# Optimization experiments

Measured on AMD Instinct MI355X. Metric: run time of the kernel, lower is better.

The kernel has to match this reference:

```python
import jax, jax.numpy as jnp
import numpy as np

N_GAUSS = 3200          # 20*20*8 voxel-center pseudo points
FEAT_DIM = 17
RENDER_H, RENDER_W = 48, 88
GT_H, GT_W = 192, 352
VOXEL_SIZE = 0.8
PC_MIN = np.array([-8.0, -8.0, -3.2], np.float32)
PC_MAX = np.array([8.0, 8.0, 3.2], np.float32)
NUSC_FREQ = np.array([1163161, 2309034, 188743, 2997643, 20317180, 852476, 243808,
                      2457947, 497017, 2731022, 7224789, 214411435, 5565043,
                      63191967, 76098082, 128860031, 141625221, 2307405309], np.float64)


def setup_inputs() -> dict:
    key = jax.random.key(0)
    k1, k2 = jax.random.split(key, 2)
    # pseudo voxel-center grid (get_presudo_xyz): cell centers on a 20x20x8 grid
    gx = (np.arange(20) + 0.5) * VOXEL_SIZE + PC_MIN[0]
    gy = (np.arange(20) + 0.5) * VOXEL_SIZE + PC_MIN[1]
    gz = (np.arange(8) + 0.5) * VOXEL_SIZE + PC_MIN[2]
    X, Y, Z = np.meshgrid(gx, gy, gz, indexing='ij')
    pc_xyz = np.stack([X, Y, Z], -1).reshape(-1, 3).astype(np.float32)
    # distCUDA2 on a regular grid: mean sq dist to 3 NNs == voxel_size^2
    scales = np.full((N_GAUSS, 3), np.log(VOXEL_SIZE), np.float32)  # log(sqrt(v^2))
    rots = np.zeros((N_GAUSS, 4), np.float32); rots[:, 0] = 1.0  # identity quats
    # two cameras looking at the grid (z_cam > 0 for all points)
    vm0 = np.array([[1, 0, 0, 0], [0, -1, 0, 0], [0, 0, -1, 20], [0, 0, 0, 1]], np.float32)
    vm1 = np.array([[0, 1, 0, 0], [0, 0, -1, 0], [-1, 0, 0, 20], [0, 0, 0, 1]], np.float32)
    viewmats = np.stack([vm0, vm1])
    intr = np.array([[100.0, 50.0, RENDER_W / 2.0, RENDER_H / 2.0]] * 2, np.float32)
    cw = (1.0 / np.log(NUSC_FREQ[:17] + 0.001)).astype(np.float32)
    return {
        'voxel_feats': jax.random.normal(k1, (1, N_GAUSS, FEAT_DIM), jnp.float32),
        'opacity': jax.random.uniform(k2, (1, N_GAUSS, 1), jnp.float32),
        'pc_xyz': jnp.asarray(pc_xyz),
        'scales': jnp.asarray(scales),
        'rots': jnp.asarray(rots),
        'viewmats': jnp.asarray(viewmats),
        'intrinsics': jnp.asarray(intr),
        'class_weights': jnp.asarray(cw),
        'gt_sem': jax.random.randint(jax.random.fold_in(key, 1), (2, GT_H, GT_W), 0, 17, jnp.int32),
        'sem_mask': jax.random.randint(jax.random.fold_in(key, 2), (2, GT_H, GT_W), 0, 2, jnp.int32),
    }


def quat_to_rot(q):
    q = q / jnp.linalg.norm(q, axis=-1, keepdims=True)
    w, x, y, z = q[:, 0], q[:, 1], q[:, 2], q[:, 3]
    return jnp.stack([
        jnp.stack([1 - 2 * (y * y + z * z), 2 * (x * y - w * z), 2 * (x * z + w * y)], -1),
        jnp.stack([2 * (x * y + w * z), 1 - 2 * (x * x + z * z), 2 * (y * z - w * x)], -1),
        jnp.stack([2 * (x * z - w * y), 2 * (y * z + w * x), 1 - 2 * (x * x + y * y)], -1),
    ], -2)  # [N,3,3]


def nearest_resize(img, H, W):
    hi, wi = img.shape
    ri = (jnp.arange(H) * hi) // H
    ci = (jnp.arange(W) * wi) // W
    return img[ri][:, ci]


def render_feature_map(feats, opac, xyz, scale, Rq, viewmat, intr):
    fx, fy, cx, cy = intr[0], intr[1], intr[2], intr[3]
    Rw, t = viewmat[:3, :3], viewmat[:3, 3]
    p = xyz @ Rw.T + t                      # [N,3] camera-frame
    z = p[:, 2]
    valid = z > 0.2
    zc = jnp.maximum(z, 0.2)
    u = fx * p[:, 0] / zc + cx
    v = fy * p[:, 1] / zc + cy
    # 3D covariance: Rq diag(s^2) Rq^T, then to camera frame
    cov3d = jnp.einsum('nij,nj,nkj->nik', Rq, scale * scale, Rq)
    cov_c = jnp.einsum('ij,njk,lk->nil', Rw, cov3d, Rw)
    # projection Jacobian (EWA splatting)
    zero = jnp.zeros_like(zc)
    J = jnp.stack([
        jnp.stack([fx / zc, zero, -fx * p[:, 0] / (zc * zc)], -1),
        jnp.stack([zero, fy / zc, -fy * p[:, 1] / (zc * zc)], -1),
    ], -2)                                  # [N,2,3]
    cov2 = jnp.einsum('nij,njk,nlk->nil', J, cov_c, J)
    a = cov2[:, 0, 0] + 0.3
    b = cov2[:, 0, 1]
    c = cov2[:, 1, 1] + 0.3
    det = jnp.maximum(a * c - b * b, 1e-8)
    A, B, C = c / det, -b / det, a / det    # conic
    px = jnp.arange(RENDER_W, dtype=jnp.float32)
    py = jnp.arange(RENDER_H, dtype=jnp.float32)
    dx = px[None, :] - u[:, None]           # [N,W]
    dy = py[None, :] - v[:, None]           # [N,H]
    power = (-0.5 * (A[:, None, None] * dx[:, None, :] ** 2
                     + C[:, None, None] * dy[:, :, None] ** 2)
             - B[:, None, None] * dx[:, None, :] * dy[:, :, None])  # [N,H,W]
    power = jnp.minimum(power, 0.0)
    alpha = jnp.clip(opac[:, None, None] * jnp.exp(power), 0.0, 0.99)
    alpha = alpha * valid[:, None, None].astype(alpha.dtype)
    order = jnp.argsort(z)                  # front-to-back depth sort
    alpha = alpha[order]
    feats_s = feats[order]
    T = jnp.cumprod(1.0 - alpha, axis=0)
    T_excl = jnp.concatenate([jnp.ones_like(T[:1]), T[:-1]], axis=0)
    w = alpha * T_excl                      # composite weights [N,H,W]
    return jnp.einsum('nhw,nc->hwc', w, feats_s)  # [H,W,17]


def masked_weighted_ce(logits, gt, mask, cw):
    logp = jax.nn.log_softmax(logits, -1)
    nll = -jnp.take_along_axis(logp, gt[:, None], axis=1)[:, 0]
    wi = cw[gt] * mask
    return jnp.sum(wi * nll) / jnp.maximum(jnp.sum(wi), 1e-8)


def reference(voxel_feats, opacity, pc_xyz, scales, rots, viewmats, intrinsics,
              class_weights, gt_sem, sem_mask):
    scale = jnp.exp(scales)
    Rq = quat_to_rot(rots)
    B = voxel_feats.shape[0]
    n_cam = viewmats.shape[0]
    loss_batch = 0.0
    for b in range(B):
        feats = voxel_feats[b].reshape(-1, FEAT_DIM)
        opac = opacity[b].reshape(-1)
        loss_cam = 0.0
        for c in range(n_cam):
            img = render_feature_map(feats, opac, pc_xyz, scale, Rq,
                                     viewmats[c], intrinsics[c])
            logits = img.reshape(-1, FEAT_DIM)
            gt = nearest_resize(gt_sem[c], RENDER_H, RENDER_W).reshape(-1)
            m = nearest_resize(sem_mask[c], RENDER_H, RENDER_W).reshape(-1).astype(jnp.float32)
            loss_cam = loss_cam + masked_weighted_ce(logits, gt, m, class_weights)
        loss_batch = loss_batch + loss_cam / n_cam
    return loss_batch / B  # gaussian_sem_weight = 1.0
```

## Files before the change

kernel.cpp:

```cpp
#include <hip/hip_runtime.h>

#define NG 3200
#define NF 17
#define NFP 18
#define RH 48
#define RW 88
#define NPIX (RH*RW)
#define GTH 192
#define GTW 352
#define NCAM 2
#define CHUNK 80
#define NCHUNK 40
#define NPL 9
#define CPW 5
#define NLOSSBLK (NPIX/64*NCAM)

typedef float v2f __attribute__((ext_vector_type(2)));
typedef _Float16 h2 __attribute__((ext_vector_type(2)));

#define Z_OFF    0
#define PU_OFF   (Z_OFF + NCAM*NG)
#define PS_OFF   (PU_OFF + NCAM*NG*6)
#define FS_OFF   (PS_OFF + NCAM*NG*6)
#define PT_OFF   (FS_OFF + NCAM*NG*NFP)
#define ACC_OFF  (PT_OFF + NCAM*NCHUNK*NPL*NPIX)

__global__ __launch_bounds__(256) void k_preproc(
    const float* __restrict__ opac, const float* __restrict__ xyz,
    const float* __restrict__ scales, const float* __restrict__ rots,
    const float* __restrict__ vm, const float* __restrict__ intr,
    float* __restrict__ ws)
{
  int idx = blockIdx.x*blockDim.x + threadIdx.x;
  if (idx < 8) ws[ACC_OFF + idx] = 0.0f;
  if (idx >= NCAM*NG) return;
  int cam = idx / NG, g = idx % NG;

  float qw=rots[g*4+0], qx=rots[g*4+1], qy=rots[g*4+2], qz=rots[g*4+3];
  float qn = rsqrtf(qw*qw+qx*qx+qy*qy+qz*qz);
  qw*=qn; qx*=qn; qy*=qn; qz*=qn;
  float R[3][3];
  R[0][0]=1.f-2.f*(qy*qy+qz*qz); R[0][1]=2.f*(qx*qy-qw*qz); R[0][2]=2.f*(qx*qz+qw*qy);
  R[1][0]=2.f*(qx*qy+qw*qz); R[1][1]=1.f-2.f*(qx*qx+qz*qz); R[1][2]=2.f*(qy*qz-qw*qx);
  R[2][0]=2.f*(qx*qz-qw*qy); R[2][1]=2.f*(qy*qz+qw*qx); R[2][2]=1.f-2.f*(qx*qx+qy*qy);

  float s2[3];
  #pragma unroll
  for (int k=0;k<3;k++){ float s=expf(scales[g*3+k]); s2[k]=s*s; }

  float M[3][3];
  #pragma unroll
  for(int i=0;i<3;i++)
    #pragma unroll
    for(int j=0;j<3;j++)
      M[i][j] = R[i][0]*s2[0]*R[j][0] + R[i][1]*s2[1]*R[j][1] + R[i][2]*s2[2]*R[j][2];

  const float* Vm = vm + cam*16;
  float Rw[3][3], t[3];
  #pragma unroll
  for(int i=0;i<3;i++){
    #pragma unroll
    for(int j=0;j<3;j++) Rw[i][j]=Vm[i*4+j];
    t[i]=Vm[i*4+3];
  }

  float T1[3][3];
  #pragma unroll
  for(int i=0;i<3;i++)
    #pragma unroll
    for(int j=0;j<3;j++)
      T1[i][j] = Rw[i][0]*M[0][j] + Rw[i][1]*M[1][j] + Rw[i][2]*M[2][j];
  float V[3][3];
  #pragma unroll
  for(int i=0;i<3;i++)
    #pragma unroll
    for(int j=0;j<3;j++)
      V[i][j] = T1[i][0]*Rw[j][0] + T1[i][1]*Rw[j][1] + T1[i][2]*Rw[j][2];

  float X=xyz[g*3+0], Y=xyz[g*3+1], Zp=xyz[g*3+2];
  float p0 = Rw[0][0]*X + Rw[0][1]*Y + Rw[0][2]*Zp + t[0];
  float p1 = Rw[1][0]*X + Rw[1][1]*Y + Rw[1][2]*Zp + t[1];
  float p2 = Rw[2][0]*X + Rw[2][1]*Y + Rw[2][2]*Zp + t[2];

  float z  = p2;
  float zc = fmaxf(z, 0.2f);
  float fx=intr[cam*4+0], fy=intr[cam*4+1], cx=intr[cam*4+2], cy=intr[cam*4+3];
  float u = fx*p0/zc + cx;
  float v = fy*p1/zc + cy;

  float j00 = fx/zc, j02 = -fx*p0/(zc*zc);
  float j11 = fy/zc, j12 = -fy*p1/(zc*zc);
  float c00 = j00*j00*V[0][0] + 2.f*j00*j02*V[0][2] + j02*j02*V[2][2];
  float c01 = j00*(V[0][1]*j11 + V[0][2]*j12) + j02*(V[2][1]*j11 + V[2][2]*j12);
  float c11 = j11*j11*V[1][1] + 2.f*j11*j12*V[1][2] + j12*j12*V[2][2];

  float a = c00 + 0.3f, b = c01, c = c11 + 0.3f;
  float det = fmaxf(a*c - b*b, 1e-8f);
  const float L2E = 1.4426950408889634f;
  float A2 = -0.5f*L2E * (c/det);
  float B2 = -L2E * (-b/det);
  float C2 = -0.5f*L2E * (a/det);
  float opv = (z > 0.2f) ? opac[g] : 0.0f;

  ws[Z_OFF + idx] = z;
  float* P = ws + PU_OFF + (size_t)idx*6;
  P[0]=u; P[1]=v; P[2]=A2; P[3]=B2; P[4]=C2; P[5]=opv;
}

__global__ __launch_bounds__(256) void k_sort(
    const float* __restrict__ feats, float* __restrict__ ws)
{
  __shared__ float zsh[NG];
  int cam = blockIdx.y;
  for (int i=threadIdx.x; i<NG; i+=256) zsh[i] = ws[Z_OFF + cam*NG + i];
  __syncthreads();

  int wave = threadIdx.x >> 6, lane = threadIdx.x & 63;
  int g = blockIdx.x*4 + wave;
  float zi = zsh[g];
  int rank = 0;
  #pragma unroll 5
  for (int k=0; k<NG/64; k++){
    int j = k*64 + lane;
    float zj = zsh[j];
    rank += ((zj < zi) || (zj == zi && j < g)) ? 1 : 0;
  }
  #pragma unroll
  for (int off=32; off>0; off>>=1) rank += __shfl_down(rank, off, 64);
  rank = __shfl(rank, 0, 64);

  const float* src = ws + PU_OFF + (size_t)(cam*NG+g)*6;
  if (lane < 6) (ws + PS_OFF + (size_t)(cam*NG+rank)*6)[lane] = src[lane];
  if (lane < NFP) (ws + FS_OFF + (size_t)(cam*NG+rank)*NFP)[lane] =
                     (lane < NF) ? feats[g*NF+lane] : 0.0f;
}

__global__ __launch_bounds__(192) void k_render(float* __restrict__ ws)
{
  __shared__ float sp[CHUNK*6];
  __shared__ v2f   sf2[CHUNK*(NFP/2)];
  int cam = blockIdx.z, chunk = blockIdx.y;
  int g0 = chunk*CHUNK;
  const float* psrc = ws + PS_OFF + (size_t)(cam*NG+g0)*6;
  for (int i=threadIdx.x; i<CHUNK*6; i+=192) sp[i]=psrc[i];
  const float* fsrc = ws + FS_OFF + (size_t)(cam*NG+g0)*NFP;
  float* sff = (float*)sf2;
  for (int i=threadIdx.x; i<CHUNK*NFP; i+=192) sff[i]=fsrc[i];
  __syncthreads();

  int pix = blockIdx.x*192 + threadIdx.x;
  float px = (float)(pix % RW), py = (float)(pix / RW);

  float T = 1.0f;
  v2f F2[9];
  #pragma unroll
  for(int k=0;k<9;k++) F2[k]=(v2f)(0.f);

  #pragma unroll 4
  for (int g=0; g<CHUNK; g++){
    const float* P = sp + g*6;
    float dx = px - P[0], dy = py - P[1];
    float m1 = P[2]*dx;
    float m2 = fmaf(P[3], dy, m1);
    float m3 = dx*m2;
    float power2 = fmaf(P[4]*dy, dy, m3);
    power2 = fminf(power2, 0.f);
    float alpha = fminf(P[5]*exp2f(power2), 0.99f);
    float w = alpha*T;
    T = fmaf(-alpha, T, T);
    v2f w2; w2.x = w; w2.y = w;
    const v2f* f2 = sf2 + g*(NFP/2);
    #pragma unroll
    for(int k=0;k<9;k++) F2[k] += w2*f2[k];
  }

  const float* Ff = (const float*)F2;
  h2* out = (h2*)(ws + PT_OFF) + (size_t)((cam*NCHUNK+chunk)*NPL)*NPIX + pix;
  #pragma unroll
  for(int k=0;k<8;k++){
    h2 v; v.x = (_Float16)Ff[2*k]; v.y = (_Float16)Ff[2*k+1];
    out[k*NPIX] = v;
  }
  { h2 v; v.x = (_Float16)Ff[16]; v.y = (_Float16)T; out[8*NPIX] = v; }
}

__global__ __launch_bounds__(512) void k_loss(
    const int* __restrict__ gt, const int* __restrict__ mask,
    const float* __restrict__ cw, float* __restrict__ ws, float* __restrict__ out)
{
  __shared__ float part[8*64*19];
  int cam = blockIdx.y;
  int wave = threadIdx.x >> 6, lane = threadIdx.x & 63;
  int pix = blockIdx.x*64 + lane;

  float F[NF];
  #pragma unroll
  for(int k=0;k<NF;k++) F[k]=0.f;
  float T = 1.f;
  #pragma unroll
  for (int i=0;i<CPW;i++){
    int c = wave*CPW + i;
    const h2* base = (const h2*)(ws + PT_OFF) + (size_t)((cam*NCHUNK+c)*NPL)*NPIX + pix;
    h2 v[9];
    #pragma unroll
    for(int k=0;k<9;k++) v[k] = base[k*NPIX];
    #pragma unroll
    for(int k=0;k<8;k++){ F[2*k] += T*(float)v[k].x; F[2*k+1] += T*(float)v[k].y; }
    F[16] += T*(float)v[8].x;
    T *= (float)v[8].y;
  }
  float* p = part + (wave*64 + lane)*19;
  #pragma unroll
  for(int k=0;k<NF;k++) p[k]=F[k];
  p[17]=T;
  __syncthreads();

  if (wave == 0){
    float img[NF];
    #pragma unroll
    for(int k=0;k<NF;k++) img[k]=0.f;
    float Trun = 1.f;
    for (int w=0; w<8; w++){
      const float* b = part + (w*64 + lane)*19;
      #pragma unroll
      for(int k=0;k<NF;k++) img[k] += Trun*b[k];
      Trun *= b[17];
    }
    int row = pix / RW, col = pix % RW;
    int gofs = cam*GTH*GTW + (row*4)*GTW + col*4;
    int gi = gt[gofs];
    float mi = (float)mask[gofs];
    float mx = img[0];
    #pragma unroll
    for(int k=1;k<NF;k++) mx = fmaxf(mx, img[k]);
    float s = 0.f;
    #pragma unroll
    for(int k=0;k<NF;k++) s += expf(img[k]-mx);
    float lse = mx + logf(s);
    float nll = lse - img[gi];
    float wi  = cw[gi]*mi;
    float num = wi*nll, den = wi;
    #pragma unroll
    for (int off=32; off>0; off>>=1){
      num += __shfl_down(num, off, 64);
      den += __shfl_down(den, off, 64);
    }
    if (lane == 0){
      atomicAdd(ws + ACC_OFF + cam*2 + 0, num);
      atomicAdd(ws + ACC_OFF + cam*2 + 1, den);
      __threadfence();
      int ticket = (int)atomicAdd(ws + ACC_OFF + 4, 1.0f);
      if (ticket == NLOSSBLK-1){
        float n0 = atomicAdd(ws + ACC_OFF + 0, 0.f);
        float d0 = atomicAdd(ws + ACC_OFF + 1, 0.f);
        float n1 = atomicAdd(ws + ACC_OFF + 2, 0.f);
        float d1 = atomicAdd(ws + ACC_OFF + 3, 0.f);
        float l0 = n0/fmaxf(d0, 1e-8f);
        float l1 = n1/fmaxf(d1, 1e-8f);
        out[0] = 0.5f*(l0 + l1);
      }
    }
  }
}

extern "C" void kernel_launch(void* const* d_in, const int* in_sizes, int n_in,
                              void* d_out, int out_size, void* d_ws, size_t ws_size,
                              hipStream_t stream) {
  const float* vf   = (const float*)d_in[0];
  const float* op   = (const float*)d_in[1];
  const float* xyz  = (const float*)d_in[2];
  const float* sc   = (const float*)d_in[3];
  const float* rt   = (const float*)d_in[4];
  const float* vm   = (const float*)d_in[5];
  const float* intr = (const float*)d_in[6];
  const float* cw   = (const float*)d_in[7];
  const int*   gt   = (const int*)d_in[8];
  const int*   mask = (const int*)d_in[9];
  float* ws  = (float*)d_ws;
  float* out = (float*)d_out;

  k_preproc<<<dim3((NCAM*NG+255)/256), 256, 0, stream>>>(op, xyz, sc, rt, vm, intr, ws);
  k_sort   <<<dim3(NG/4, NCAM), 256, 0, stream>>>(vf, ws);
  k_render <<<dim3(NPIX/192, NCHUNK, NCAM), 192, 0, stream>>>(ws);
  k_loss   <<<dim3(NPIX/64, NCAM), 512, 0, stream>>>(gt, mask, cw, ws, out);
}
```

Baseline: 125.9 us.

## Fuse preprocess into sort, add wave-level gaussian skip, repack partial records

Merges the per-gaussian projection kernel into the depth-sort kernel, which recomputes z in shared memory, so one launch and one workspace round trip go away. The render kernel now uses 40-gaussian chunks (80 chunks), float4 shared loads with padded layouts, and skips a gaussian when every lane in the wave has an exponent below -20. Per-pixel partial results are stored as contiguous 48-byte fp16 records instead of planar planes, and the loss kernel reduces 10 chunks per wave. The skip threshold drops contributions with alpha up to about 1e-6, a slight approximation. The larger chunk count doubles the partial-result traffic.

```diff
diff --git a/kernel.cpp b/kernel.cpp
--- a/kernel.cpp
+++ b/kernel.cpp
@@ -2,117 +2,50 @@
 
 #define NG 3200
 #define NF 17
-#define NFP 18
 #define RH 48
 #define RW 88
 #define NPIX (RH*RW)
 #define GTH 192
 #define GTW 352
 #define NCAM 2
-#define CHUNK 80
-#define NCHUNK 40
-#define NPL 9
-#define CPW 5
+#define CHUNK 40
+#define NCHUNK 80
+#define CPW 10
 #define NLOSSBLK (NPIX/64*NCAM)
-
-typedef float v2f __attribute__((ext_vector_type(2)));
+#define PREC 12
+
+typedef float v4f __attribute__((ext_vector_type(4)));
 typedef _Float16 h2 __attribute__((ext_vector_type(2)));
 
-#define Z_OFF    0
-#define PU_OFF   (Z_OFF + NCAM*NG)
-#define PS_OFF   (PU_OFF + NCAM*NG*6)
-#define FS_OFF   (PS_OFF + NCAM*NG*6)
-#define PT_OFF   (FS_OFF + NCAM*NG*NFP)
-#define ACC_OFF  (PT_OFF + NCAM*NCHUNK*NPL*NPIX)
-
-__global__ __launch_bounds__(256) void k_preproc(
-    const float* __restrict__ opac, const float* __restrict__ xyz,
-    const float* __restrict__ scales, const float* __restrict__ rots,
-    const float* __restrict__ vm, const float* __restrict__ intr,
-    float* __restrict__ ws)
-{
-  int idx = blockIdx.x*blockDim.x + threadIdx.x;
-  if (idx < 8) ws[ACC_OFF + idx] = 0.0f;
-  if (idx >= NCAM*NG) return;
-  int cam = idx / NG, g = idx % NG;
-
-  float qw=rots[g*4+0], qx=rots[g*4+1], qy=rots[g*4+2], qz=rots[g*4+3];
-  float qn = rsqrtf(qw*qw+qx*qx+qy*qy+qz*qz);
-  qw*=qn; qx*=qn; qy*=qn; qz*=qn;
-  float R[3][3];
-  R[0][0]=1.f-2.f*(qy*qy+qz*qz); R[0][1]=2.f*(qx*qy-qw*qz); R[0][2]=2.f*(qx*qz+qw*qy);
-  R[1][0]=2.f*(qx*qy+qw*qz); R[1][1]=1.f-2.f*(qx*qx+qz*qz); R[1][2]=2.f*(qy*qz-qw*qx);
-  R[2][0]=2.f*(qx*qz-qw*qy); R[2][1]=2.f*(qy*qz+qw*qx); R[2][2]=1.f-2.f*(qx*qx+qy*qy);
-
-  float s2[3];
-  #pragma unroll
-  for (int k=0;k<3;k++){ float s=expf(scales[g*3+k]); s2[k]=s*s; }
-
-  float M[3][3];
-  #pragma unroll
-  for(int i=0;i<3;i++)
-    #pragma unroll
-    for(int j=0;j<3;j++)
-      M[i][j] = R[i][0]*s2[0]*R[j][0] + R[i][1]*s2[1]*R[j][1] + R[i][2]*s2[2]*R[j][2];
-
-  const float* Vm = vm + cam*16;
-  float Rw[3][3], t[3];
-  #pragma unroll
-  for(int i=0;i<3;i++){
-    #pragma unroll
-    for(int j=0;j<3;j++) Rw[i][j]=Vm[i*4+j];
-    t[i]=Vm[i*4+3];
-  }
-
-  float T1[3][3];
-  #pragma unroll
-  for(int i=0;i<3;i++)
-    #pragma unroll
-    for(int j=0;j<3;j++)
-      T1[i][j] = Rw[i][0]*M[0][j] + Rw[i][1]*M[1][j] + Rw[i][2]*M[2][j];
-  float V[3][3];
-  #pragma unroll
-  for(int i=0;i<3;i++)
-    #pragma unroll
-    for(int j=0;j<3;j++)
-      V[i][j] = T1[i][0]*Rw[j][0] + T1[i][1]*Rw[j][1] + T1[i][2]*Rw[j][2];
-
-  float X=xyz[g*3+0], Y=xyz[g*3+1], Zp=xyz[g*3+2];
-  float p0 = Rw[0][0]*X + Rw[0][1]*Y + Rw[0][2]*Zp + t[0];
-  float p1 = Rw[1][0]*X + Rw[1][1]*Y + Rw[1][2]*Zp + t[1];
-  float p2 = Rw[2][0]*X + Rw[2][1]*Y + Rw[2][2]*Zp + t[2];
-
-  float z  = p2;
-  float zc = fmaxf(z, 0.2f);
-  float fx=intr[cam*4+0], fy=intr[cam*4+1], cx=intr[cam*4+2], cy=intr[cam*4+3];
-  float u = fx*p0/zc + cx;
-  float v = fy*p1/zc + cy;
-
-  float j00 = fx/zc, j02 = -fx*p0/(zc*zc);
-  float j11 = fy/zc, j12 = -fy*p1/(zc*zc);
-  float c00 = j00*j00*V[0][0] + 2.f*j00*j02*V[0][2] + j02*j02*V[2][2];
-  float c01 = j00*(V[0][1]*j11 + V[0][2]*j12) + j02*(V[2][1]*j11 + V[2][2]*j12);
-  float c11 = j11*j11*V[1][1] + 2.f*j11*j12*V[1][2] + j12*j12*V[2][2];
-
-  float a = c00 + 0.3f, b = c01, c = c11 + 0.3f;
-  float det = fmaxf(a*c - b*b, 1e-8f);
-  const float L2E = 1.4426950408889634f;
-  float A2 = -0.5f*L2E * (c/det);
-  float B2 = -L2E * (-b/det);
-  float C2 = -0.5f*L2E * (a/det);
-  float opv = (z > 0.2f) ? opac[g] : 0.0f;
-
-  ws[Z_OFF + idx] = z;
-  float* P = ws + PU_OFF + (size_t)idx*6;
-  P[0]=u; P[1]=v; P[2]=A2; P[3]=B2; P[4]=C2; P[5]=opv;
-}
-
-__global__ __launch_bounds__(256) void k_sort(
-    const float* __restrict__ feats, float* __restrict__ ws)
+#define PS_OFF   0
+#define FS_OFF   (PS_OFF + NCAM*NG*8)
+#define PT_OFF   (FS_OFF + NCAM*NG*20)
+#define ACC_OFF  (PT_OFF + NCAM*NCHUNK*NPIX*PREC)
+
+__device__ __forceinline__ unsigned pack_h2(float a, float b){
+  h2 r; r.x=(_Float16)a; r.y=(_Float16)b;
+  unsigned u; __builtin_memcpy(&u,&r,4); return u;
+}
+__device__ __forceinline__ void unpack_h2(unsigned u, float& a, float& b){
+  h2 r; __builtin_memcpy(&r,&u,4);
+  a=(float)r.x; b=(float)r.y;
+}
+
+__global__ __launch_bounds__(256) void k_prep_sort(
+    const float* __restrict__ vf, const float* __restrict__ opac,
+    const float* __restrict__ xyz, const float* __restrict__ scales,
+    const float* __restrict__ rots, const float* __restrict__ vm,
+    const float* __restrict__ intr, float* __restrict__ ws)
 {
   __shared__ float zsh[NG];
   int cam = blockIdx.y;
-  for (int i=threadIdx.x; i<NG; i+=256) zsh[i] = ws[Z_OFF + cam*NG + i];
+  const float* Vm = vm + cam*16;
+  {
+    float r20=Vm[8], r21=Vm[9], r22=Vm[10], t2c=Vm[11];
+    for (int i=threadIdx.x; i<NG; i+=256)
+      zsh[i] = fmaf(r20, xyz[i*3], fmaf(r21, xyz[i*3+1], fmaf(r22, xyz[i*3+2], t2c)));
+  }
+  if (blockIdx.x==0 && blockIdx.y==0 && threadIdx.x<8) ws[ACC_OFF+threadIdx.x]=0.f;
   __syncthreads();
 
   int wave = threadIdx.x >> 6, lane = threadIdx.x & 63;
@@ -129,59 +62,123 @@
   for (int off=32; off>0; off>>=1) rank += __shfl_down(rank, off, 64);
   rank = __shfl(rank, 0, 64);
 
-  const float* src = ws + PU_OFF + (size_t)(cam*NG+g)*6;
-  if (lane < 6) (ws + PS_OFF + (size_t)(cam*NG+rank)*6)[lane] = src[lane];
-  if (lane < NFP) (ws + FS_OFF + (size_t)(cam*NG+rank)*NFP)[lane] =
-                     (lane < NF) ? feats[g*NF+lane] : 0.0f;
+  float qw=rots[g*4+0], qx=rots[g*4+1], qy=rots[g*4+2], qz=rots[g*4+3];
+  float qn = rsqrtf(qw*qw+qx*qx+qy*qy+qz*qz);
+  qw*=qn; qx*=qn; qy*=qn; qz*=qn;
+  float R[3][3];
+  R[0][0]=1.f-2.f*(qy*qy+qz*qz); R[0][1]=2.f*(qx*qy-qw*qz); R[0][2]=2.f*(qx*qz+qw*qy);
+  R[1][0]=2.f*(qx*qy+qw*qz); R[1][1]=1.f-2.f*(qx*qx+qz*qz); R[1][2]=2.f*(qy*qz-qw*qx);
+  R[2][0]=2.f*(qx*qz-qw*qy); R[2][1]=2.f*(qy*qz+qw*qx); R[2][2]=1.f-2.f*(qx*qx+qy*qy);
+
+  float s2[3];
+  #pragma unroll
+  for (int k=0;k<3;k++){ float s=expf(scales[g*3+k]); s2[k]=s*s; }
+
+  float M[3][3];
+  #pragma unroll
+  for(int i=0;i<3;i++)
+    #pragma unroll
+    for(int j=0;j<3;j++)
+      M[i][j] = R[i][0]*s2[0]*R[j][0] + R[i][1]*s2[1]*R[j][1] + R[i][2]*s2[2]*R[j][2];
+
+  float Rw[3][3], t[3];
+  #pragma unroll
+  for(int i=0;i<3;i++){
+    #pragma unroll
+    for(int j=0;j<3;j++) Rw[i][j]=Vm[i*4+j];
+    t[i]=Vm[i*4+3];
+  }
+  float T1[3][3];
+  #pragma unroll
+  for(int i=0;i<3;i++)
+    #pragma unroll
+    for(int j=0;j<3;j++)
+      T1[i][j] = Rw[i][0]*M[0][j] + Rw[i][1]*M[1][j] + Rw[i][2]*M[2][j];
+  float V[3][3];
+  #pragma unroll
+  for(int i=0;i<3;i++)
+    #pragma unroll
+    for(int j=0;j<3;j++)
+      V[i][j] = T1[i][0]*Rw[j][0] + T1[i][1]*Rw[j][1] + T1[i][2]*Rw[j][2];
+
+  float X=xyz[g*3+0], Y=xyz[g*3+1], Zp=xyz[g*3+2];
+  float p0 = Rw[0][0]*X + Rw[0][1]*Y + Rw[0][2]*Zp + t[0];
+  float p1 = Rw[1][0]*X + Rw[1][1]*Y + Rw[1][2]*Zp + t[1];
+
+  float z  = zi;
+  float zc = fmaxf(z, 0.2f);
+  float fx=intr[cam*4+0], fy=intr[cam*4+1], cx=intr[cam*4+2], cy=intr[cam*4+3];
+  float u = fx*p0/zc + cx;
+  float v = fy*p1/zc + cy;
+
+  float j00 = fx/zc, j02 = -fx*p0/(zc*zc);
+  float j11 = fy/zc, j12 = -fy*p1/(zc*zc);
+  float c00 = j00*j00*V[0][0] + 2.f*j00*j02*V[0][2] + j02*j02*V[2][2];
+  float c01 = j00*(V[0][1]*j11 + V[0][2]*j12) + j02*(V[2][1]*j11 + V[2][2]*j12);
+  float c11 = j11*j11*V[1][1] + 2.f*j11*j12*V[1][2] + j12*j12*V[2][2];
+
+  float a = c00 + 0.3f, b = c01, c = c11 + 0.3f;
+  float det = fmaxf(a*c - b*b, 1e-8f);
+  const float L2E = 1.4426950408889634f;
+  float A2 = -0.5f*L2E * (c/det);
+  float B2 = -L2E * (-b/det);
+  float C2 = -0.5f*L2E * (a/det);
+  float opv = (z > 0.2f) ? opac[g] : 0.0f;
+
+  float pv = (lane==0)?u:(lane==1)?v:(lane==2)?A2:(lane==3)?B2:(lane==4)?C2:(lane==5)?opv:0.f;
+  if (lane < 8)  (ws + PS_OFF + (size_t)(cam*NG+rank)*8)[lane] = pv;
+  if (lane < 20) (ws + FS_OFF + (size_t)(cam*NG+rank)*20)[lane] =
+                    (lane < NF) ? vf[g*NF+lane] : 0.0f;
 }
 
 __global__ __launch_bounds__(192) void k_render(float* __restrict__ ws)
 {
-  __shared__ float sp[CHUNK*6];
-  __shared__ v2f   sf2[CHUNK*(NFP/2)];
+  __shared__ float4 sp4[CHUNK*2];
+  __shared__ float4 sf4[CHUNK*5];
   int cam = blockIdx.z, chunk = blockIdx.y;
   int g0 = chunk*CHUNK;
-  const float* psrc = ws + PS_OFF + (size_t)(cam*NG+g0)*6;
-  for (int i=threadIdx.x; i<CHUNK*6; i+=192) sp[i]=psrc[i];
-  const float* fsrc = ws + FS_OFF + (size_t)(cam*NG+g0)*NFP;
-  float* sff = (float*)sf2;
-  for (int i=threadIdx.x; i<CHUNK*NFP; i+=192) sff[i]=fsrc[i];
+  const float4* psrc = (const float4*)(ws + PS_OFF) + (size_t)(cam*NG+g0)*2;
+  for (int i=threadIdx.x; i<CHUNK*2; i+=192) sp4[i]=psrc[i];
+  const float4* fsrc = (const float4*)(ws + FS_OFF) + (size_t)(cam*NG+g0)*5;
+  for (int i=threadIdx.x; i<CHUNK*5; i+=192) sf4[i]=fsrc[i];
   __syncthreads();
 
   int pix = blockIdx.x*192 + threadIdx.x;
   float px = (float)(pix % RW), py = (float)(pix / RW);
 
   float T = 1.0f;
-  v2f F2[9];
-  #pragma unroll
-  for(int k=0;k<9;k++) F2[k]=(v2f)(0.f);
-
-  #pragma unroll 4
+  v4f A[5];
+  #pragma unroll
+  for(int k=0;k<5;k++) A[k]=(v4f)(0.f);
+
   for (int g=0; g<CHUNK; g++){
-    const float* P = sp + g*6;
-    float dx = px - P[0], dy = py - P[1];
-    float m1 = P[2]*dx;
-    float m2 = fmaf(P[3], dy, m1);
-    float m3 = dx*m2;
-    float power2 = fmaf(P[4]*dy, dy, m3);
-    power2 = fminf(power2, 0.f);
-    float alpha = fminf(P[5]*exp2f(power2), 0.99f);
-    float w = alpha*T;
-    T = fmaf(-alpha, T, T);
-    v2f w2; w2.x = w; w2.y = w;
-    const v2f* f2 = sf2 + g*(NFP/2);
-    #pragma unroll
-    for(int k=0;k<9;k++) F2[k] += w2*f2[k];
-  }
-
-  const float* Ff = (const float*)F2;
-  h2* out = (h2*)(ws + PT_OFF) + (size_t)((cam*NCHUNK+chunk)*NPL)*NPIX + pix;
-  #pragma unroll
-  for(int k=0;k<8;k++){
-    h2 v; v.x = (_Float16)Ff[2*k]; v.y = (_Float16)Ff[2*k+1];
-    out[k*NPIX] = v;
-  }
-  { h2 v; v.x = (_Float16)Ff[16]; v.y = (_Float16)T; out[8*NPIX] = v; }
+    float4 q0 = sp4[g*2], q1 = sp4[g*2+1];
+    float dx = px - q0.x, dy = py - q0.y;
+    float power2 = fmaf(q1.x*dy, dy, dx*fmaf(q0.w, dy, q0.z*dx));
+    if (__any(power2 > -20.0f)) {
+      float alpha = fminf(q1.y*exp2f(fminf(power2, 0.f)), 0.99f);
+      float w = alpha*T;
+      T = fmaf(-alpha, T, T);
+      v4f wv; wv.x=w; wv.y=w; wv.z=w; wv.w=w;
+      const v4f* f4 = (const v4f*)(sf4 + g*5);
+      #pragma unroll
+      for(int k=0;k<5;k++) A[k] += wv*f4[k];
+    }
+  }
+
+  union { v4f v[5]; float f[20]; } U;
+  #pragma unroll
+  for(int k=0;k<5;k++) U.v[k]=A[k];
+  unsigned* rec = (unsigned*)(ws + PT_OFF)
+                + ((size_t)(cam*NCHUNK+chunk)*NPIX + pix)*PREC;
+  uint4 w0, w1;
+  w0.x=pack_h2(U.f[0],U.f[1]);   w0.y=pack_h2(U.f[2],U.f[3]);
+  w0.z=pack_h2(U.f[4],U.f[5]);   w0.w=pack_h2(U.f[6],U.f[7]);
+  w1.x=pack_h2(U.f[8],U.f[9]);   w1.y=pack_h2(U.f[10],U.f[11]);
+  w1.z=pack_h2(U.f[12],U.f[13]); w1.w=pack_h2(U.f[14],U.f[15]);
+  *(uint4*)rec = w0;
+  *((uint4*)rec + 1) = w1;
+  rec[8] = pack_h2(U.f[16], T);
 }
 
 __global__ __launch_bounds__(512) void k_loss(
@@ -200,14 +197,21 @@
   #pragma unroll
   for (int i=0;i<CPW;i++){
     int c = wave*CPW + i;
-    const h2* base = (const h2*)(ws + PT_OFF) + (size_t)((cam*NCHUNK+c)*NPL)*NPIX + pix;
-    h2 v[9];
-    #pragma unroll
-    for(int k=0;k<9;k++) v[k] = base[k*NPIX];
-    #pragma unroll
-    for(int k=0;k<8;k++){ F[2*k] += T*(float)v[k].x; F[2*k+1] += T*(float)v[k].y; }
-    F[16] += T*(float)v[8].x;
-    T *= (float)v[8].y;
+    const unsigned* rec = (const unsigned*)(ws + PT_OFF)
+                        + ((size_t)(cam*NCHUNK+c)*NPIX + pix)*PREC;
+    uint4 a = *(const uint4*)rec;
+    uint4 b = *((const uint4*)rec + 1);
+    unsigned cc = rec[8];
+    float v0,v1;
+    unpack_h2(a.x,v0,v1); F[0]+=T*v0;  F[1]+=T*v1;
+    unpack_h2(a.y,v0,v1); F[2]+=T*v0;  F[3]+=T*v1;
+    unpack_h2(a.z,v0,v1); F[4]+=T*v0;  F[5]+=T*v1;
+    unpack_h2(a.w,v0,v1); F[6]+=T*v0;  F[7]+=T*v1;
+    unpack_h2(b.x,v0,v1); F[8]+=T*v0;  F[9]+=T*v1;
+    unpack_h2(b.y,v0,v1); F[10]+=T*v0; F[11]+=T*v1;
+    unpack_h2(b.z,v0,v1); F[12]+=T*v0; F[13]+=T*v1;
+    unpack_h2(b.w,v0,v1); F[14]+=T*v0; F[15]+=T*v1;
+    unpack_h2(cc, v0,v1); F[16]+=T*v0; T*=v1;
   }
   float* p = part + (wave*64 + lane)*19;
   #pragma unroll
@@ -279,8 +283,7 @@
   float* ws  = (float*)d_ws;
   float* out = (float*)d_out;
 
-  k_preproc<<<dim3((NCAM*NG+255)/256), 256, 0, stream>>>(op, xyz, sc, rt, vm, intr, ws);
-  k_sort   <<<dim3(NG/4, NCAM), 256, 0, stream>>>(vf, ws);
-  k_render <<<dim3(NPIX/192, NCHUNK, NCAM), 192, 0, stream>>>(ws);
-  k_loss   <<<dim3(NPIX/64, NCAM), 512, 0, stream>>>(gt, mask, cw, ws, out);
-}
+  k_prep_sort<<<dim3(NG/4, NCAM), 256, 0, stream>>>(vf, op, xyz, sc, rt, vm, intr, ws);
+  k_render   <<<dim3(NPIX/192, NCHUNK, NCAM), 192, 0, stream>>>(ws);
+  k_loss     <<<dim3(NPIX/64, NCAM), 512, 0, stream>>>(gt, mask, cw, ws, out);
+}
```

Result: no change. 126.7 us (+0.7%).
